# Performance work log

Measured on AMD Instinct MI355X. Metric: run time of the kernel, lower is better.

The kernel has to match this reference:

```python
import jax, jax.numpy as jnp
import numpy as np

B, V, E, H, L = 8, 200, 40000, 128, 3


def setup_inputs() -> dict:
    key = jax.random.key(0)
    ks = jax.random.split(key, 24)
    s = 1.0 / np.sqrt(H)
    inp = {
        "x": jax.random.normal(ks[0], (B, V, 2), jnp.float32),
        "e": jax.random.uniform(ks[1], (B, E), jnp.float32),
        "edge_index": jax.random.randint(ks[2], (B, 2, E), 0, V),
        # Embedder
        "node_W": jax.random.normal(ks[3], (2, H), jnp.float32) * 0.5,
        "node_b": jnp.zeros((H,), jnp.float32),
        "edge_W": jax.random.normal(ks[4], (1, H), jnp.float32) * 0.5,
        "edge_b": jnp.zeros((H,), jnp.float32),
        # GCN layers (stacked over L)
        "U_W": jax.random.normal(ks[5], (L, H, H), jnp.float32) * s,
        "U_b": jnp.zeros((L, H), jnp.float32),
        "V_W": jax.random.normal(ks[6], (L, H, H), jnp.float32) * s,
        "V_b": jnp.zeros((L, H), jnp.float32),
        "A_W": jax.random.normal(ks[7], (L, H, H), jnp.float32) * s,
        "A_b": jnp.zeros((L, H), jnp.float32),
        "B_W": jax.random.normal(ks[8], (L, H, H), jnp.float32) * s,
        "B_b": jnp.zeros((L, H), jnp.float32),
        "C_W": jax.random.normal(ks[9], (L, H, H), jnp.float32) * s,
        "C_b": jnp.zeros((L, H), jnp.float32),
        # Out MLP: hidden -> hidden -> 2
        "out_W1": jax.random.normal(ks[10], (H, H), jnp.float32) * s,
        "out_b1": jnp.zeros((H,), jnp.float32),
        "out_W2": jax.random.normal(ks[11], (H, 2), jnp.float32) * s,
        "out_b2": jnp.zeros((2,), jnp.float32),
    }
    return inp


def reference(x, e, edge_index, node_W, node_b, edge_W, edge_b,
              U_W, U_b, V_W, V_b, A_W, A_b, B_W, B_b, C_W, C_b,
              out_W1, out_b1, out_W2, out_b2):
    n_nodes = x.shape[1]
    n_layers = U_W.shape[0]

    def per_graph(xi, ei, idx):
        # Embedder: coords (V,2)->(V,H), distances (E,)->(E,H)
        xh = xi @ node_W + node_b
        eh = ei[:, None] @ edge_W + edge_b
        src, dst = idx[0], idx[1]
        for l in range(n_layers):
            gate = jax.nn.sigmoid(eh)                       # (E,H) edge gates
            vx = xh @ V_W[l] + V_b[l]                       # (V,H)
            agg = jax.ops.segment_sum(gate * vx[src], dst,
                                      num_segments=n_nodes)  # (V,H)
            x_new = xh + jax.nn.relu(xh @ U_W[l] + U_b[l] + agg)
            eh = eh + jax.nn.relu(eh @ A_W[l] + A_b[l]
                                  + (xh @ B_W[l] + B_b[l])[src]
                                  + (xh @ C_W[l] + C_b[l])[dst])
            xh = x_new
        h = jax.nn.relu(eh @ out_W1 + out_b1)
        return jax.nn.sigmoid(h @ out_W2 + out_b2)           # (E,2)

    # batch loop in the original torch code -> vmap here
    return jax.vmap(per_graph)(x, e, edge_index)
```

## Files before the change

### kernel.cpp

```cpp
#include <hip/hip_runtime.h>
#include <hip/hip_bf16.h>

#define NB 8
#define NV 200
#define NE 40000
#define NH 128
#define NL 3
#define EBLK 313

typedef __attribute__((ext_vector_type(8))) __bf16 bf16x8;
typedef __attribute__((ext_vector_type(8))) short s16x8;
typedef __attribute__((ext_vector_type(4))) float f32x4;

__device__ inline float sigmoidf_(float x){ return 1.0f/(1.0f + __expf(-x)); }

__device__ inline short f2b(float f){
  union{ float f; unsigned u; } v; v.f = f;
  unsigned u = v.u;
  u += 0x7fffu + ((u >> 16) & 1u);
  return (short)(u >> 16);
}
__device__ inline float b2f(short s){
  union{ unsigned u; float f; } v; v.u = ((unsigned)(unsigned short)s) << 16;
  return v.f;
}
__device__ inline void splitb(float x, short &hi, short &lo){
  hi = f2b(x);
  lo = f2b(x - b2f(hi));
}

__global__ __launch_bounds__(256) void k_embed_nodes(
    const float* __restrict__ x, const float* __restrict__ nW,
    const float* __restrict__ nb, float* __restrict__ xh)
{
  int i = blockIdx.x*256 + threadIdx.x;
  if (i >= NB*NV*NH) return;
  int h  = i & (NH-1);
  int bv = i >> 7;
  xh[i] = x[bv*2+0]*nW[h] + x[bv*2+1]*nW[NH+h] + nb[h];
}

__global__ __launch_bounds__(256) void k_trans_w(
    const float* __restrict__ AW, const float* __restrict__ oW1,
    short* __restrict__ Wt)
{
  int m = blockIdx.x;
  const float* src = (m < 3) ? (AW + m*NH*NH) : oW1;
  short* dhi = Wt + (size_t)m*NH*NH;
  short* dlo = Wt + (size_t)(4+m)*NH*NH;
  for (int i = threadIdx.x; i < NH*NH; i += 256){
    int n = i >> 7, k = i & 127;
    short hi, lo;
    splitb(src[k*NH + n], hi, lo);
    dhi[i] = hi; dlo[i] = lo;
  }
}

__global__ __launch_bounds__(256) void k_zero(int* __restrict__ p, int n){
  int i = blockIdx.x*256 + threadIdx.x;
  if (i < n) p[i] = 0;
}

__global__ __launch_bounds__(256) void k_count(const int* __restrict__ ei, int* __restrict__ counts){
  int i = blockIdx.x*256 + threadIdx.x;
  if (i >= NB*NE) return;
  int b = i / NE, e = i % NE;
  int dv = ei[b*2*NE + NE + e];
  atomicAdd(&counts[b*NV + dv], 1);
}

__global__ void k_scan(const int* __restrict__ counts, int* __restrict__ offs, int* __restrict__ cursor){
  int b = blockIdx.x;
  if (threadIdx.x == 0){
    int run = 0;
    for (int v=0; v<NV; v++){
      offs[b*(NV+1)+v] = run;
      cursor[b*NV+v]   = run;
      run += counts[b*NV+v];
    }
    offs[b*(NV+1)+NV] = run;
  }
}

__global__ __launch_bounds__(256) void k_scatter(const int* __restrict__ ei, int* __restrict__ cursor, int* __restrict__ csr){
  int i = blockIdx.x*256 + threadIdx.x;
  if (i >= NB*NE) return;
  int b = i / NE, e = i % NE;
  int dv = ei[b*2*NE + NE + e];
  int pos = atomicAdd(&cursor[b*NV + dv], 1);
  csr[(size_t)b*NE + pos] = e;
}

__global__ __launch_bounds__(256) void k_node_mm(
    float* __restrict__ xh, const float* __restrict__ agg,
    const float* __restrict__ VWl, const float* __restrict__ Vbl,
    const float* __restrict__ BWl, const float* __restrict__ Bbl,
    const float* __restrict__ CWl, const float* __restrict__ Cbl,
    const float* __restrict__ UWl, const float* __restrict__ Ubl,
    float* __restrict__ vx, float* __restrict__ bx,
    float* __restrict__ cx, float* __restrict__ ux,
    int do_update)
{
  __shared__ float sx[NH];
  int b = blockIdx.x / NV, v = blockIdx.x % NV;
  size_t row = (size_t)b*NV + v;
  float* xr = xh + row*NH;
  int ht = threadIdx.x;
  if (ht < NH){
    float xv = xr[ht];
    if (do_update){
      float u = ux[row*NH + ht] + agg[row*NH + ht] + agg[(size_t)NB*NV*NH + row*NH + ht];
      xv += u > 0.f ? u : 0.f;
      xr[ht] = xv;
    }
    sx[ht] = xv;
  }
  __syncthreads();
  #pragma unroll
  for (int pass=0; pass<2; pass++){
    int t = threadIdx.x + pass*256;
    int mat = t >> 7, h = t & 127;
    const float* W = (mat==0) ? VWl : (mat==1) ? BWl : (mat==2) ? CWl : UWl;
    const float* bs = (mat==0) ? Vbl : (mat==1) ? Bbl : (mat==2) ? Cbl : Ubl;
    float* op = (mat==0) ? vx : (mat==1) ? bx : (mat==2) ? cx : ux;
    float acc = bs[h];
    #pragma unroll 8
    for (int k=0;k<NH;k++) acc += sx[k]*W[k*NH + h];
    op[row*NH + h] = acc;
  }
}

__global__ __launch_bounds__(128) void k_agg(
    const float* __restrict__ eh, const float* __restrict__ evec,
    const float* __restrict__ eWe, const float* __restrict__ ebe,
    const float* __restrict__ vx, const int* __restrict__ ei,
    const int* __restrict__ csr, const int* __restrict__ offs,
    float* __restrict__ agg, int is_l0)
{
  int part = blockIdx.x & 1;
  int bv   = blockIdx.x >> 1;
  int b = bv / NV, v = bv % NV;
  int h = threadIdx.x;
  const int* srcp  = ei + b*2*NE;
  const int* csrg  = csr + (size_t)b*NE;
  const float* ehg = eh + (size_t)b*NE*NH;
  const float* evg = evec + (size_t)b*NE;
  const float* vxg = vx + (size_t)b*NV*NH;
  float wh = eWe[h], bh = ebe[h];
  int beg = offs[b*(NV+1)+v], end = offs[b*(NV+1)+v+1];
  int mid = (beg + end) >> 1;
  int i    = part ? mid : beg;
  int stop = part ? end : mid;
  float acc = 0.f;
  for (; i+8 <= stop; i += 8){
    int   eb[8], sb[8];
    float a[8], w[8];
    #pragma unroll
    for (int j=0;j<8;j++) eb[j] = csrg[i+j];
    #pragma unroll
    for (int j=0;j<8;j++) sb[j] = srcp[eb[j]];
    if (is_l0){
      #pragma unroll
      for (int j=0;j<8;j++) a[j] = evg[eb[j]]*wh + bh;
    } else {
      #pragma unroll
      for (int j=0;j<8;j++) a[j] = ehg[(size_t)eb[j]*NH + h];
    }
    #pragma unroll
    for (int j=0;j<8;j++) w[j] = vxg[sb[j]*NH + h];
    #pragma unroll
    for (int j=0;j<8;j++) acc += sigmoidf_(a[j]) * w[j];
  }
  for (; i < stop; i++){
    int e0 = csrg[i]; int s0 = srcp[e0];
    float a = is_l0 ? (evg[e0]*wh + bh) : ehg[(size_t)e0*NH+h];
    acc += sigmoidf_(a) * vxg[s0*NH+h];
  }
  agg[((size_t)part*NB*NV + (size_t)b*NV + v)*NH + h] = acc;
}

__global__ __launch_bounds__(256) void k_edge_update(
    float* __restrict__ eh, const short* __restrict__ Wt,
    const float* __restrict__ Ab, const float* __restrict__ bx,
    const float* __restrict__ cx, const int* __restrict__ ei,
    const float* __restrict__ evec, const float* __restrict__ eWe,
    const float* __restrict__ ebe, int is_l0)
{
  __shared__ short sW[2*NH*NH];
  const short* Whi = Wt;
  const short* Wlo = Wt + 4*NH*NH;
  {
    #pragma unroll
    for (int i=0;i<16;i++){
      int sidx = (threadIdx.x + i*256)*8;
      int p = sidx >> 14, r = sidx & 16383;
      int hh = r >> 7, kw = r & 127;
      const short* src = p ? Wlo : Whi;
      s16x8 vv = *(const s16x8*)(src + r);
      *(s16x8*)(sW + p*16384 + hh*128 + (kw ^ ((hh&7)<<3))) = vv;
    }
  }
  __syncthreads();

  int blk  = blockIdx.x % EBLK;
  int b    = blockIdx.x / EBLK;
  int wave = threadIdx.x >> 6;
  int lane = threadIdx.x & 63;
  int l15 = lane & 15, lg = lane >> 4;
  int eA = blk*128 + wave*32 + l15;
  int eB = eA + 16;
  int eAc = eA < NE ? eA : NE-1;
  int eBc = eB < NE ? eB : NE-1;
  float* ehg = eh + (size_t)b*NE*NH;
  const int* srcp = ei + b*2*NE;
  int svA = srcp[eAc], dvA = srcp[NE+eAc];
  int svB = srcp[eBc], dvB = srcp[NE+eBc];

  float evA = 0.f, evB = 0.f;
  f32x4 rA[8], rB[8];
  if (is_l0){
    evA = evec[(size_t)b*NE + eAc];
    evB = evec[(size_t)b*NE + eBc];
    #pragma unroll
    for (int kk=0;kk<4;kk++){
      f32x4 w0 = *(const f32x4*)(eWe + kk*32 + lg*8);
      f32x4 w1 = *(const f32x4*)(eWe + kk*32 + lg*8 + 4);
      f32x4 q0 = *(const f32x4*)(ebe + kk*32 + lg*8);
      f32x4 q1 = *(const f32x4*)(ebe + kk*32 + lg*8 + 4);
      #pragma unroll
      for (int j=0;j<4;j++){
        rA[2*kk][j]   = evA*w0[j] + q0[j];
        rA[2*kk+1][j] = evA*w1[j] + q1[j];
        rB[2*kk][j]   = evB*w0[j] + q0[j];
        rB[2*kk+1][j] = evB*w1[j] + q1[j];
      }
    }
  } else {
    const float* pA = ehg + (size_t)eAc*NH + lg*8;
    const float* pB = ehg + (size_t)eBc*NH + lg*8;
    #pragma unroll
    for (int kk=0;kk<4;kk++){
      rA[2*kk]   = *(const f32x4*)(pA + kk*32);
      rA[2*kk+1] = *(const f32x4*)(pA + kk*32 + 4);
    }
    #pragma unroll
    for (int kk=0;kk<4;kk++){
      rB[2*kk]   = *(const f32x4*)(pB + kk*32);
      rB[2*kk+1] = *(const f32x4*)(pB + kk*32 + 4);
    }
  }

  bf16x8 ahA[4], alA[4], ahB[4], alB[4];
  #pragma unroll
  for (int kk=0;kk<4;kk++){
    union{ short s[8]; bf16x8 v; } uh, ul;
    #pragma unroll
    for (int j=0;j<4;j++){
      splitb(rA[2*kk][j],   uh.s[j],   ul.s[j]);
      splitb(rA[2*kk+1][j], uh.s[4+j], ul.s[4+j]);
    }
    ahA[kk] = uh.v; alA[kk] = ul.v;
  }
  #pragma unroll
  for (int kk=0;kk<4;kk++){
    union{ short s[8]; bf16x8 v; } uh, ul;
    #pragma unroll
    for (int j=0;j<4;j++){
      splitb(rB[2*kk][j],   uh.s[j],   ul.s[j]);
      splitb(rB[2*kk+1][j], uh.s[4+j], ul.s[4+j]);
    }
    ahB[kk] = uh.v; alB[kk] = ul.v;
  }

  f32x4 accA[8], accB[8];
  #pragma unroll
  for (int n=0;n<8;n++){ accA[n] = (f32x4){0.f,0.f,0.f,0.f}; accB[n] = (f32x4){0.f,0.f,0.f,0.f}; }

  #pragma unroll
  for (int kk=0;kk<4;kk++){
    #pragma unroll
    for (int n=0;n<8;n++){
      int row = n*16 + l15;
      int cofs = (kk*32 + lg*8) ^ ((l15&7)<<3);
      union{ s16x8 s; bf16x8 v; } wh, wl;
      wh.s = *(const s16x8*)(sW + row*128 + cofs);
      wl.s = *(const s16x8*)(sW + 16384 + row*128 + cofs);
      accA[n] = __builtin_amdgcn_mfma_f32_16x16x32_bf16(wh.v, ahA[kk], accA[n], 0, 0, 0);
      accA[n] = __builtin_amdgcn_mfma_f32_16x16x32_bf16(wh.v, alA[kk], accA[n], 0, 0, 0);
      accA[n] = __builtin_amdgcn_mfma_f32_16x16x32_bf16(wl.v, ahA[kk], accA[n], 0, 0, 0);
      accB[n] = __builtin_amdgcn_mfma_f32_16x16x32_bf16(wh.v, ahB[kk], accB[n], 0, 0, 0);
      accB[n] = __builtin_amdgcn_mfma_f32_16x16x32_bf16(wh.v, alB[kk], accB[n], 0, 0, 0);
      accB[n] = __builtin_amdgcn_mfma_f32_16x16x32_bf16(wl.v, ahB[kk], accB[n], 0, 0, 0);
    }
  }

  const float* bxA = bx + ((size_t)b*NV + svA)*NH;
  const float* cxA = cx + ((size_t)b*NV + dvA)*NH;
  const float* bxB = bx + ((size_t)b*NV + svB)*NH;
  const float* cxB = cx + ((size_t)b*NV + dvB)*NH;
  float* ehA = ehg + (size_t)eAc*NH;
  float* ehB = ehg + (size_t)eBc*NH;
  #pragma unroll
  for (int n=0;n<8;n++){
    int h0 = n*16 + lg*4;
    f32x4 ab4 = *(const f32x4*)(Ab + h0);
    f32x4 bA = *(const f32x4*)(bxA + h0);
    f32x4 cA = *(const f32x4*)(cxA + h0);
    f32x4 bB = *(const f32x4*)(bxB + h0);
    f32x4 cB = *(const f32x4*)(cxB + h0);
    f32x4 oA, oB;
    if (is_l0){
      f32x4 w4 = *(const f32x4*)(eWe + h0);
      f32x4 q4 = *(const f32x4*)(ebe + h0);
      #pragma unroll
      for (int j=0;j<4;j++){ oA[j] = evA*w4[j] + q4[j]; oB[j] = evB*w4[j] + q4[j]; }
    } else {
      oA = *(const f32x4*)(ehA + h0);
      oB = *(const f32x4*)(ehB + h0);
    }
    f32x4 nA, nB;
    #pragma unroll
    for (int j=0;j<4;j++){
      float vA = accA[n][j] + ab4[j] + bA[j] + cA[j];
      vA = vA > 0.f ? vA : 0.f;
      nA[j] = oA[j] + vA;
      float vB = accB[n][j] + ab4[j] + bB[j] + cB[j];
      vB = vB > 0.f ? vB : 0.f;
      nB[j] = oB[j] + vB;
    }
    if (eA < NE) *(f32x4*)(ehA + h0) = nA;
    if (eB < NE) *(f32x4*)(ehB + h0) = nB;
  }
}

__global__ __launch_bounds__(256) void k_out(
    const float* __restrict__ eh, const short* __restrict__ Wt,
    const float* __restrict__ b1, const float* __restrict__ W2,
    const float* __restrict__ b2, float* __restrict__ out)
{
  __shared__ short sW[2*NH*NH];
  const short* Whi = Wt + 3*NH*NH;
  const short* Wlo = Wt + 7*NH*NH;
  {
    #pragma unroll
    for (int i=0;i<16;i++){
      int sidx = (threadIdx.x + i*256)*8;
      int p = sidx >> 14, r = sidx & 16383;
      int hh = r >> 7, kw = r & 127;
      const short* src = p ? Wlo : Whi;
      s16x8 vv = *(const s16x8*)(src + r);
      *(s16x8*)(sW + p*16384 + hh*128 + (kw ^ ((hh&7)<<3))) = vv;
    }
  }
  __syncthreads();

  int blk  = blockIdx.x % EBLK;
  int b    = blockIdx.x / EBLK;
  int wave = threadIdx.x >> 6;
  int lane = threadIdx.x & 63;
  int l15 = lane & 15, lg = lane >> 4;
  int eA = blk*128 + wave*32 + l15;
  int eB = eA + 16;
  int eAc = eA < NE ? eA : NE-1;
  int eBc = eB < NE ? eB : NE-1;
  const float* ehg = eh + (size_t)b*NE*NH;

  const float* pA = ehg + (size_t)eAc*NH + lg*8;
  const float* pB = ehg + (size_t)eBc*NH + lg*8;
  f32x4 rA[8], rB[8];
  #pragma unroll
  for (int kk=0;kk<4;kk++){
    rA[2*kk]   = *(const f32x4*)(pA + kk*32);
    rA[2*kk+1] = *(const f32x4*)(pA + kk*32 + 4);
  }
  #pragma unroll
  for (int kk=0;kk<4;kk++){
    rB[2*kk]   = *(const f32x4*)(pB + kk*32);
    rB[2*kk+1] = *(const f32x4*)(pB + kk*32 + 4);
  }

  bf16x8 ahA[4], alA[4], ahB[4], alB[4];
  #pragma unroll
  for (int kk=0;kk<4;kk++){
    union{ short s[8]; bf16x8 v; } uh, ul;
    #pragma unroll
    for (int j=0;j<4;j++){
      splitb(rA[2*kk][j],   uh.s[j],   ul.s[j]);
      splitb(rA[2*kk+1][j], uh.s[4+j], ul.s[4+j]);
    }
    ahA[kk] = uh.v; alA[kk] = ul.v;
  }
  #pragma unroll
  for (int kk=0;kk<4;kk++){
    union{ short s[8]; bf16x8 v; } uh, ul;
    #pragma unroll
    for (int j=0;j<4;j++){
      splitb(rB[2*kk][j],   uh.s[j],   ul.s[j]);
      splitb(rB[2*kk+1][j], uh.s[4+j], ul.s[4+j]);
    }
    ahB[kk] = uh.v; alB[kk] = ul.v;
  }

  f32x4 accA[8], accB[8];
  #pragma unroll
  for (int n=0;n<8;n++){ accA[n] = (f32x4){0.f,0.f,0.f,0.f}; accB[n] = (f32x4){0.f,0.f,0.f,0.f}; }
  #pragma unroll
  for (int kk=0;kk<4;kk++){
    #pragma unroll
    for (int n=0;n<8;n++){
      int row = n*16 + l15;
      int cofs = (kk*32 + lg*8) ^ ((l15&7)<<3);
      union{ s16x8 s; bf16x8 v; } wh, wl;
      wh.s = *(const s16x8*)(sW + row*128 + cofs);
      wl.s = *(const s16x8*)(sW + 16384 + row*128 + cofs);
      accA[n] = __builtin_amdgcn_mfma_f32_16x16x32_bf16(wh.v, ahA[kk], accA[n], 0, 0, 0);
      accA[n] = __builtin_amdgcn_mfma_f32_16x16x32_bf16(wh.v, alA[kk], accA[n], 0, 0, 0);
      accA[n] = __builtin_amdgcn_mfma_f32_16x16x32_bf16(wl.v, ahA[kk], accA[n], 0, 0, 0);
      accB[n] = __builtin_amdgcn_mfma_f32_16x16x32_bf16(wh.v, ahB[kk], accB[n], 0, 0, 0);
      accB[n] = __builtin_amdgcn_mfma_f32_16x16x32_bf16(wh.v, alB[kk], accB[n], 0, 0, 0);
      accB[n] = __builtin_amdgcn_mfma_f32_16x16x32_bf16(wl.v, ahB[kk], accB[n], 0, 0, 0);
    }
  }

  float p0A = 0.f, p1A = 0.f, p0B = 0.f, p1B = 0.f;
  #pragma unroll
  for (int n=0;n<8;n++){
    int h0 = n*16 + lg*4;
    f32x4 b14 = *(const f32x4*)(b1 + h0);
    f32x4 wA  = *(const f32x4*)(W2 + h0*2);
    f32x4 wB  = *(const f32x4*)(W2 + h0*2 + 4);
    #pragma unroll
    for (int j=0;j<4;j++){
      float w20 = (j<2) ? wA[2*j]   : wB[2*(j-2)];
      float w21 = (j<2) ? wA[2*j+1] : wB[2*(j-2)+1];
      float hA = accA[n][j] + b14[j]; hA = hA > 0.f ? hA : 0.f;
      float hB = accB[n][j] + b14[j]; hB = hB > 0.f ? hB : 0.f;
      p0A += hA*w20; p1A += hA*w21;
      p0B += hB*w20; p1B += hB*w21;
    }
  }
  p0A += __shfl_xor(p0A, 16, 64); p0A += __shfl_xor(p0A, 32, 64);
  p1A += __shfl_xor(p1A, 16, 64); p1A += __shfl_xor(p1A, 32, 64);
  p0B += __shfl_xor(p0B, 16, 64); p0B += __shfl_xor(p0B, 32, 64);
  p1B += __shfl_xor(p1B, 16, 64); p1B += __shfl_xor(p1B, 32, 64);
  if (lg == 0){
    float bb0 = b2[0], bb1 = b2[1];
    if (eA < NE){
      float2 r; r.x = sigmoidf_(p0A + bb0); r.y = sigmoidf_(p1A + bb1);
      *(float2*)(out + ((size_t)b*NE + eA)*2) = r;
    }
    if (eB < NE){
      float2 r; r.x = sigmoidf_(p0B + bb0); r.y = sigmoidf_(p1B + bb1);
      *(float2*)(out + ((size_t)b*NE + eB)*2) = r;
    }
  }
}

extern "C" void kernel_launch(void* const* d_in, const int* in_sizes, int n_in,
                              void* d_out, int out_size, void* d_ws, size_t ws_size,
                              hipStream_t stream)
{
  const float* x   = (const float*)d_in[0];
  const float* e   = (const float*)d_in[1];
  const int*   ei  = (const int*)d_in[2];
  const float* nW  = (const float*)d_in[3];
  const float* nb  = (const float*)d_in[4];
  const float* eW  = (const float*)d_in[5];
  const float* eb  = (const float*)d_in[6];
  const float* UW  = (const float*)d_in[7];
  const float* Ub  = (const float*)d_in[8];
  const float* VW  = (const float*)d_in[9];
  const float* Vb  = (const float*)d_in[10];
  const float* AW  = (const float*)d_in[11];
  const float* Ab  = (const float*)d_in[12];
  const float* BW  = (const float*)d_in[13];
  const float* Bb  = (const float*)d_in[14];
  const float* CW  = (const float*)d_in[15];
  const float* Cb  = (const float*)d_in[16];
  const float* oW1 = (const float*)d_in[17];
  const float* ob1 = (const float*)d_in[18];
  const float* oW2 = (const float*)d_in[19];
  const float* ob2 = (const float*)d_in[20];
  float* out = (float*)d_out;

  char* ws = (char*)d_ws;
  size_t off = 0;
  auto alloc = [&](size_t bytes)->char*{
    char* p = ws + off;
    off += (bytes + 255) & ~(size_t)255;
    return p;
  };
  float* eh     = (float*)alloc((size_t)NB*NE*NH*4);
  float* xh     = (float*)alloc((size_t)NB*NV*NH*4);
  float* vx     = (float*)alloc((size_t)NB*NV*NH*4);
  float* bx     = (float*)alloc((size_t)NB*NV*NH*4);
  float* cx     = (float*)alloc((size_t)NB*NV*NH*4);
  float* ux     = (float*)alloc((size_t)NB*NV*NH*4);
  float* agg    = (float*)alloc((size_t)2*NB*NV*NH*4);
  short* Wt     = (short*)alloc((size_t)8*NH*NH*2);
  int* counts   = (int*)alloc((size_t)NB*NV*4);
  int* cursor   = (int*)alloc((size_t)NB*NV*4);
  int* offs     = (int*)alloc((size_t)NB*(NV+1)*4);
  int* csr      = (int*)alloc((size_t)NB*NE*4);
  (void)ws_size; (void)in_sizes; (void)n_in; (void)out_size;

  k_embed_nodes<<<(NB*NV*NH+255)/256, 256, 0, stream>>>(x, nW, nb, xh);
  k_trans_w<<<4, 256, 0, stream>>>(AW, oW1, Wt);
  k_zero<<<(NB*NV+255)/256, 256, 0, stream>>>(counts, NB*NV);
  k_count<<<(NB*NE+255)/256, 256, 0, stream>>>(ei, counts);
  k_scan<<<NB, 64, 0, stream>>>(counts, offs, cursor);
  k_scatter<<<(NB*NE+255)/256, 256, 0, stream>>>(ei, cursor, csr);

  for (int l=0; l<NL; l++){
    k_node_mm<<<NB*NV, 256, 0, stream>>>(xh, agg,
        VW + l*NH*NH, Vb + l*NH, BW + l*NH*NH, Bb + l*NH,
        CW + l*NH*NH, Cb + l*NH, UW + l*NH*NH, Ub + l*NH,
        vx, bx, cx, ux, l > 0 ? 1 : 0);
    if (l < NL-1)
      k_agg<<<NB*NV*2, 128, 0, stream>>>(eh, e, eW, eb, vx, ei, csr, offs, agg, l==0 ? 1 : 0);
    k_edge_update<<<NB*EBLK, 256, 0, stream>>>(eh, Wt + l*NH*NH, Ab + l*NH, bx, cx, ei,
                                               e, eW, eb, l==0 ? 1 : 0);
  }
  k_out<<<NB*EBLK, 256, 0, stream>>>(eh, Wt, ob1, oW2, ob2, out);
}
```

Measured before the change: 554.9 us.

## Fuse last edge update with output MLP, enlarge edge blocks, split aggregation four ways

The final layer's edge update is merged into the output kernel, so the updated edge features stay in registers and go straight into the out_W1 MFMA. This avoids writing the full edge tensor to memory and reading it back. Edge kernels now run 512 threads over 256 edges per block, halving the number of weight staging loads into LDS. Node aggregation is split into four partial sums instead of two to raise parallelism, at the cost of more partial buffers to sum.

```diff
diff --git a/kernel.cpp b/kernel.cpp
--- a/kernel.cpp
+++ b/kernel.cpp
@@ -6,10 +6,11 @@
 #define NE 40000
 #define NH 128
 #define NL 3
-#define EBLK 313
+#define EBLK 157
 
 typedef __attribute__((ext_vector_type(8))) __bf16 bf16x8;
 typedef __attribute__((ext_vector_type(8))) short s16x8;
+typedef __attribute__((ext_vector_type(4))) short s16x4;
 typedef __attribute__((ext_vector_type(4))) float f32x4;
 
 __device__ inline float sigmoidf_(float x){ return 1.0f/(1.0f + __expf(-x)); }
@@ -109,7 +110,9 @@
   if (ht < NH){
     float xv = xr[ht];
     if (do_update){
-      float u = ux[row*NH + ht] + agg[row*NH + ht] + agg[(size_t)NB*NV*NH + row*NH + ht];
+      float u = ux[row*NH + ht];
+      #pragma unroll
+      for (int p=0;p<4;p++) u += agg[(size_t)p*NB*NV*NH + row*NH + ht];
       xv += u > 0.f ? u : 0.f;
       xr[ht] = xv;
     }
@@ -137,8 +140,8 @@
     const int* __restrict__ csr, const int* __restrict__ offs,
     float* __restrict__ agg, int is_l0)
 {
-  int part = blockIdx.x & 1;
-  int bv   = blockIdx.x >> 1;
+  int part = blockIdx.x & 3;
+  int bv   = blockIdx.x >> 2;
   int b = bv / NV, v = bv % NV;
   int h = threadIdx.x;
   const int* srcp  = ei + b*2*NE;
@@ -148,9 +151,9 @@
   const float* vxg = vx + (size_t)b*NV*NH;
   float wh = eWe[h], bh = ebe[h];
   int beg = offs[b*(NV+1)+v], end = offs[b*(NV+1)+v+1];
-  int mid = (beg + end) >> 1;
-  int i    = part ? mid : beg;
-  int stop = part ? end : mid;
+  int len = end - beg;
+  int i    = beg + ((len*part) >> 2);
+  int stop = beg + ((len*(part+1)) >> 2);
   float acc = 0.f;
   for (; i+8 <= stop; i += 8){
     int   eb[8], sb[8];
@@ -179,7 +182,7 @@
   agg[((size_t)part*NB*NV + (size_t)b*NV + v)*NH + h] = acc;
 }
 
-__global__ __launch_bounds__(256) void k_edge_update(
+__global__ __launch_bounds__(512) void k_edge_update(
     float* __restrict__ eh, const short* __restrict__ Wt,
     const float* __restrict__ Ab, const float* __restrict__ bx,
     const float* __restrict__ cx, const int* __restrict__ ei,
@@ -191,8 +194,8 @@
   const short* Wlo = Wt + 4*NH*NH;
   {
     #pragma unroll
-    for (int i=0;i<16;i++){
-      int sidx = (threadIdx.x + i*256)*8;
+    for (int i=0;i<8;i++){
+      int sidx = (threadIdx.x + i*512)*8;
       int p = sidx >> 14, r = sidx & 16383;
       int hh = r >> 7, kw = r & 127;
       const short* src = p ? Wlo : Whi;
@@ -207,7 +210,7 @@
   int wave = threadIdx.x >> 6;
   int lane = threadIdx.x & 63;
   int l15 = lane & 15, lg = lane >> 4;
-  int eA = blk*128 + wave*32 + l15;
+  int eA = blk*256 + wave*32 + l15;
   int eB = eA + 16;
   int eAc = eA < NE ? eA : NE-1;
   int eBc = eB < NE ? eB : NE-1;
@@ -333,18 +336,20 @@
   }
 }
 
-__global__ __launch_bounds__(256) void k_out(
+__global__ __launch_bounds__(512) void k_edge_out(
     const float* __restrict__ eh, const short* __restrict__ Wt,
+    const float* __restrict__ Ab, const float* __restrict__ bx,
+    const float* __restrict__ cx, const int* __restrict__ ei,
     const float* __restrict__ b1, const float* __restrict__ W2,
     const float* __restrict__ b2, float* __restrict__ out)
 {
   __shared__ short sW[2*NH*NH];
-  const short* Whi = Wt + 3*NH*NH;
-  const short* Wlo = Wt + 7*NH*NH;
+  const short* Whi = Wt + 2*NH*NH;
+  const short* Wlo = Wt + 6*NH*NH;
   {
     #pragma unroll
-    for (int i=0;i<16;i++){
-      int sidx = (threadIdx.x + i*256)*8;
+    for (int i=0;i<8;i++){
+      int sidx = (threadIdx.x + i*512)*8;
       int p = sidx >> 14, r = sidx & 16383;
       int hh = r >> 7, kw = r & 127;
       const short* src = p ? Wlo : Whi;
@@ -359,11 +364,14 @@
   int wave = threadIdx.x >> 6;
   int lane = threadIdx.x & 63;
   int l15 = lane & 15, lg = lane >> 4;
-  int eA = blk*128 + wave*32 + l15;
+  int eA = blk*256 + wave*32 + l15;
   int eB = eA + 16;
   int eAc = eA < NE ? eA : NE-1;
   int eBc = eB < NE ? eB : NE-1;
   const float* ehg = eh + (size_t)b*NE*NH;
+  const int* srcp = ei + b*2*NE;
+  int svA = srcp[eAc], dvA = srcp[NE+eAc];
+  int svB = srcp[eBc], dvB = srcp[NE+eBc];
 
   const float* pA = ehg + (size_t)eAc*NH + lg*8;
   const float* pB = ehg + (size_t)eBc*NH + lg*8;
@@ -422,6 +430,87 @@
     }
   }
 
+  f32x4 nAr[8], nBr[8];
+  const float* bxA = bx + ((size_t)b*NV + svA)*NH;
+  const float* cxA = cx + ((size_t)b*NV + dvA)*NH;
+  const float* bxB = bx + ((size_t)b*NV + svB)*NH;
+  const float* cxB = cx + ((size_t)b*NV + dvB)*NH;
+  const float* ehA = ehg + (size_t)eAc*NH;
+  const float* ehB = ehg + (size_t)eBc*NH;
+  #pragma unroll
+  for (int n=0;n<8;n++){
+    int h0 = n*16 + lg*4;
+    f32x4 ab4 = *(const f32x4*)(Ab + h0);
+    f32x4 bA = *(const f32x4*)(bxA + h0);
+    f32x4 cA = *(const f32x4*)(cxA + h0);
+    f32x4 oA = *(const f32x4*)(ehA + h0);
+    f32x4 bB = *(const f32x4*)(bxB + h0);
+    f32x4 cB = *(const f32x4*)(cxB + h0);
+    f32x4 oB = *(const f32x4*)(ehB + h0);
+    #pragma unroll
+    for (int j=0;j<4;j++){
+      float vA = accA[n][j] + ab4[j] + bA[j] + cA[j];
+      vA = vA > 0.f ? vA : 0.f;
+      nAr[n][j] = oA[j] + vA;
+      float vB = accB[n][j] + ab4[j] + bB[j] + cB[j];
+      vB = vB > 0.f ? vB : 0.f;
+      nBr[n][j] = oB[j] + vB;
+    }
+  }
+
+  __syncthreads();
+  {
+    const short* W1hi = Wt + 3*NH*NH;
+    const short* W1lo = Wt + 7*NH*NH;
+    #pragma unroll
+    for (int i=0;i<16;i++){
+      int qd = threadIdx.x + i*512;
+      int p = qd >> 12, rr = qd & 4095;
+      int row = rr >> 5;
+      int c0 = (rr & 31) << 2;
+      int kk = c0 >> 5, lgs = (c0 >> 3) & 3, jhi = (c0 & 7) >> 2;
+      int base = 32*kk + 16*jhi + 4*lgs;
+      const short* src = p ? W1lo : W1hi;
+      s16x4 v = *(const s16x4*)(src + row*128 + base);
+      *(s16x4*)(sW + p*16384 + row*128 + (c0 ^ ((row&7)<<3))) = v;
+    }
+  }
+  __syncthreads();
+
+  bf16x8 qhA[4], qlA[4], qhB[4], qlB[4];
+  #pragma unroll
+  for (int kk=0;kk<4;kk++){
+    union{ short s[8]; bf16x8 v; } uhA, ulA, uhB, ulB;
+    #pragma unroll
+    for (int j=0;j<8;j++){
+      splitb(nAr[2*kk + (j>>2)][j&3], uhA.s[j], ulA.s[j]);
+      splitb(nBr[2*kk + (j>>2)][j&3], uhB.s[j], ulB.s[j]);
+    }
+    qhA[kk] = uhA.v; qlA[kk] = ulA.v;
+    qhB[kk] = uhB.v; qlB[kk] = ulB.v;
+  }
+
+  f32x4 acc2A[8], acc2B[8];
+  #pragma unroll
+  for (int n=0;n<8;n++){ acc2A[n] = (f32x4){0.f,0.f,0.f,0.f}; acc2B[n] = (f32x4){0.f,0.f,0.f,0.f}; }
+  #pragma unroll
+  for (int kk=0;kk<4;kk++){
+    #pragma unroll
+    for (int n=0;n<8;n++){
+      int row = n*16 + l15;
+      int cofs = (kk*32 + lg*8) ^ ((l15&7)<<3);
+      union{ s16x8 s; bf16x8 v; } wh, wl;
+      wh.s = *(const s16x8*)(sW + row*128 + cofs);
+      wl.s = *(const s16x8*)(sW + 16384 + row*128 + cofs);
+      acc2A[n] = __builtin_amdgcn_mfma_f32_16x16x32_bf16(wh.v, qhA[kk], acc2A[n], 0, 0, 0);
+      acc2A[n] = __builtin_amdgcn_mfma_f32_16x16x32_bf16(wh.v, qlA[kk], acc2A[n], 0, 0, 0);
+      acc2A[n] = __builtin_amdgcn_mfma_f32_16x16x32_bf16(wl.v, qhA[kk], acc2A[n], 0, 0, 0);
+      acc2B[n] = __builtin_amdgcn_mfma_f32_16x16x32_bf16(wh.v, qhB[kk], acc2B[n], 0, 0, 0);
+      acc2B[n] = __builtin_amdgcn_mfma_f32_16x16x32_bf16(wh.v, qlB[kk], acc2B[n], 0, 0, 0);
+      acc2B[n] = __builtin_amdgcn_mfma_f32_16x16x32_bf16(wl.v, qhB[kk], acc2B[n], 0, 0, 0);
+    }
+  }
+
   float p0A = 0.f, p1A = 0.f, p0B = 0.f, p1B = 0.f;
   #pragma unroll
   for (int n=0;n<8;n++){
@@ -433,8 +522,8 @@
     for (int j=0;j<4;j++){
       float w20 = (j<2) ? wA[2*j]   : wB[2*(j-2)];
       float w21 = (j<2) ? wA[2*j+1] : wB[2*(j-2)+1];
-      float hA = accA[n][j] + b14[j]; hA = hA > 0.f ? hA : 0.f;
-      float hB = accB[n][j] + b14[j]; hB = hB > 0.f ? hB : 0.f;
+      float hA = acc2A[n][j] + b14[j]; hA = hA > 0.f ? hA : 0.f;
+      float hB = acc2B[n][j] + b14[j]; hB = hB > 0.f ? hB : 0.f;
       p0A += hA*w20; p1A += hA*w21;
       p0B += hB*w20; p1B += hB*w21;
     }
@@ -496,7 +585,7 @@
   float* bx     = (float*)alloc((size_t)NB*NV*NH*4);
   float* cx     = (float*)alloc((size_t)NB*NV*NH*4);
   float* ux     = (float*)alloc((size_t)NB*NV*NH*4);
-  float* agg    = (float*)alloc((size_t)2*NB*NV*NH*4);
+  float* agg    = (float*)alloc((size_t)4*NB*NV*NH*4);
   short* Wt     = (short*)alloc((size_t)8*NH*NH*2);
   int* counts   = (int*)alloc((size_t)NB*NV*4);
   int* cursor   = (int*)alloc((size_t)NB*NV*4);
@@ -517,9 +606,12 @@
         CW + l*NH*NH, Cb + l*NH, UW + l*NH*NH, Ub + l*NH,
         vx, bx, cx, ux, l > 0 ? 1 : 0);
     if (l < NL-1)
-      k_agg<<<NB*NV*2, 128, 0, stream>>>(eh, e, eW, eb, vx, ei, csr, offs, agg, l==0 ? 1 : 0);
-    k_edge_update<<<NB*EBLK, 256, 0, stream>>>(eh, Wt + l*NH*NH, Ab + l*NH, bx, cx, ei,
-                                               e, eW, eb, l==0 ? 1 : 0);
-  }
-  k_out<<<NB*EBLK, 256, 0, stream>>>(eh, Wt, ob1, oW2, ob2, out);
-}
+      k_agg<<<NB*NV*4, 128, 0, stream>>>(eh, e, eW, eb, vx, ei, csr, offs, agg, l==0 ? 1 : 0);
+    if (l < NL-1)
+      k_edge_update<<<NB*EBLK, 512, 0, stream>>>(eh, Wt + l*NH*NH, Ab + l*NH, bx, cx, ei,
+                                                 e, eW, eb, l==0 ? 1 : 0);
+    else
+      k_edge_out<<<NB*EBLK, 512, 0, stream>>>(eh, Wt, Ab + l*NH, bx, cx, ei,
+                                              ob1, oW2, ob2, out);
+  }
+}
```

Measured after the change: 554.7 us. No clear change (-0.0%).
